# Optimization experiments

Measured on AMD Instinct MI355X. Metric: run time of the kernel, lower is better.

The kernel has to match this reference:

```python
import jax, jax.numpy as jnp
import numpy as np

S, B, D, E, H, REQ = 2048, 4, 256, 256, 8, 16  # seq, batch, hidden_dim, embed(=hidden_size), heads, band half-width


def setup_inputs() -> dict:
    key = jax.random.key(0)
    ks = jax.random.split(key, 12)
    w = lambda k, shape: jax.random.normal(k, shape, jnp.float32) * 0.02
    return {
        "mod": jax.random.normal(ks[0], (S, B, D), jnp.float32),
        "mask": jnp.zeros((B, S), jnp.float32),  # unused in speaker=False branch (kept for fidelity)
        "Wq": w(ks[1], (E, D)), "bq": jnp.zeros((E,), jnp.float32),
        "Wk": w(ks[2], (E, D)), "bk": jnp.zeros((E,), jnp.float32),
        "Wv": w(ks[3], (E, D)), "bv": jnp.zeros((E,), jnp.float32),
        "Win": w(ks[4], (3 * E, E)), "bin_": jnp.zeros((3 * E,), jnp.float32),  # MHA in_proj
        "Wout": w(ks[5], (E, E)), "bout": jnp.zeros((E,), jnp.float32),         # MHA out_proj
        "Wfc": w(ks[6], (D, E)), "bfc": jnp.zeros((D,), jnp.float32),           # self.fc
        "gamma": jnp.ones((D,), jnp.float32), "beta": jnp.zeros((D,), jnp.float32),
        "req": REQ,
    }


def reference(mod, mask, Wq, bq, Wk, bk, Wv, bv, Win, bin_, Wout, bout, Wfc, bfc, gamma, beta, req):
    s, b, d = mod.shape
    e = Wq.shape[0]
    hd = e // H
    # fc_q/k/v (pre-projection) then MultiheadAttention's own in_proj
    q = mod @ Wq.T + bq                       # (s, b, e)
    k = mod @ Wk.T + bk
    v = mod @ Wv.T + bv
    q = q @ Win[:e].T + bin_[:e]
    k = k @ Win[e:2 * e].T + bin_[e:2 * e]
    v = v @ Win[2 * e:].T + bin_[2 * e:]
    split = lambda x: x.reshape(s, b, H, hd).transpose(1, 2, 0, 3)  # (b, H, s, hd)
    qh, kh, vh = split(q), split(k), split(v)
    scores = jnp.einsum('bhqd,bhkd->bhqk', qh, kh) / jnp.sqrt(jnp.float32(hd))
    idx = jnp.arange(s)
    allowed = jnp.abs(idx[:, None] - idx[None, :]) < req  # band: diag + offsets 1..req-1
    scores = jnp.where(allowed[None, None], scores, -jnp.inf)
    attn = jax.nn.softmax(scores, axis=-1)                # attn dropout = identity (eval)
    ctx = jnp.einsum('bhqk,bhkd->bhqd', attn, vh)
    ctx = ctx.transpose(2, 0, 1, 3).reshape(s, b, e)
    ctx = ctx @ Wout.T + bout
    y = ctx @ Wfc.T + bfc + mod                           # dropout(0.5) = identity (eval), residual
    mu = jnp.mean(y, axis=-1, keepdims=True)
    var = jnp.var(y, axis=-1, keepdims=True)
    return (y - mu) / jnp.sqrt(var + 1e-6) * gamma + beta
```

## Files before the change

### kernel.cpp

```cpp
#include <hip/hip_runtime.h>
#include <hip/hip_bf16.h>
#include <math.h>

#define SS 2048
#define BB 4
#define DD 256
#define EE 256
#define HH 8
#define HD 32
#define TT (SS*BB)

typedef unsigned short ushortt;
typedef __attribute__((ext_vector_type(8))) short short8;
typedef __attribute__((ext_vector_type(4))) float f32x4;

__device__ __forceinline__ float bfbits2f(ushortt u) {
    return __uint_as_float(((unsigned int)u) << 16);
}
__device__ __forceinline__ ushortt f2bf_bits(float f) {
    unsigned int u = __float_as_uint(f);
    unsigned int r = u + 0x7FFFu + ((u >> 16) & 1u);
    return (ushortt)(r >> 16);
}

__device__ __forceinline__ int robust_req(const void* p) {
    int i = *(const int*)p;
    if (i >= 1 && i <= SS) return i;
    float f = __int_as_float(i);
    if (f >= 1.f && f <= (float)SS) return (int)(f + 0.5f);
    float b = bfbits2f(*(const ushortt*)p);
    if (b >= 1.f && b <= (float)SS) return (int)(b + 0.5f);
    return 16;
}

__global__ __launch_bounds__(256)
void fuse_weights(const float* __restrict__ Win,
                  const float* __restrict__ Wq, const float* __restrict__ Wk,
                  const float* __restrict__ Wv,
                  const float* __restrict__ bq, const float* __restrict__ bk,
                  const float* __restrict__ bv, const float* __restrict__ bin_,
                  const float* __restrict__ Wfc, const float* __restrict__ Wout,
                  const float* __restrict__ bout, const float* __restrict__ bfc,
                  ushortt* __restrict__ Weffb, float* __restrict__ beff,
                  ushortt* __restrict__ W2b, float* __restrict__ b2) {
    __shared__ float red[4];
    int t = threadIdx.x;
    if (blockIdx.x < 3 * EE) {
        int r = blockIdx.x;
        int i = r / EE;
        const float* Wi = (i == 0) ? Wq : ((i == 1) ? Wk : Wv);
        const float* bi = (i == 0) ? bq : ((i == 1) ? bk : bv);
        float acc = 0.f;
        for (int e1 = 0; e1 < EE; ++e1) acc += Win[r * EE + e1] * Wi[e1 * DD + t];
        Weffb[(size_t)r * DD + t] = f2bf_bits(acc);
        float tb = Win[r * EE + t] * bi[t];
#pragma unroll
        for (int off = 32; off >= 1; off >>= 1) tb += __shfl_xor(tb, off);
        if ((t & 63) == 0) red[t >> 6] = tb;
        __syncthreads();
        if (t == 0) beff[r] = red[0] + red[1] + red[2] + red[3] + bin_[r];
    } else {
        int d = blockIdx.x - 3 * EE;
        float acc = 0.f;
        for (int e = 0; e < EE; ++e) acc += Wfc[d * EE + e] * Wout[e * EE + t];
        W2b[(size_t)d * EE + t] = f2bf_bits(acc);
        float tb = Wfc[d * EE + t] * bout[t];
#pragma unroll
        for (int off = 32; off >= 1; off >>= 1) tb += __shfl_xor(tb, off);
        if ((t & 63) == 0) red[t >> 6] = tb;
        __syncthreads();
        if (t == 0) b2[d] = red[0] + red[1] + red[2] + red[3] + bfc[d];
    }
}

__global__ __launch_bounds__(256)
void gemm_qkv(const float* __restrict__ A, const ushortt* __restrict__ Bw,
              const float* __restrict__ bias, ushortt* __restrict__ C,
              int M, int N, int K) {
    __shared__ __align__(16) ushortt Alds[128][40];
    __shared__ __align__(16) ushortt Blds[64][40];
    const int t    = threadIdx.x;
    const int lane = t & 63;
    const int w    = t >> 6;
    const int wm   = w >> 1, wn = w & 1;
    const int quad = lane >> 4;
    const int l16  = lane & 15;
    const int m0   = blockIdx.y * 128;
    const int n0   = blockIdx.x * 64;

    f32x4 acc[4][2];
#pragma unroll
    for (int fm = 0; fm < 4; ++fm)
#pragma unroll
        for (int fn = 0; fn < 2; ++fn) acc[fm][fn] = (f32x4){0.f, 0.f, 0.f, 0.f};

    const int sr = t >> 2;
    const int sp = (t & 3) * 8;

    for (int k0 = 0; k0 < K; k0 += 32) {
#pragma unroll
        for (int half = 0; half < 2; ++half) {
            const float* ap = A + (size_t)(m0 + sr + half * 64) * K + k0 + sp;
            float4 v0 = *(const float4*)ap;
            float4 v1 = *(const float4*)(ap + 4);
            ushort4 o0, o1;
            o0.x = f2bf_bits(v0.x); o0.y = f2bf_bits(v0.y);
            o0.z = f2bf_bits(v0.z); o0.w = f2bf_bits(v0.w);
            o1.x = f2bf_bits(v1.x); o1.y = f2bf_bits(v1.y);
            o1.z = f2bf_bits(v1.z); o1.w = f2bf_bits(v1.w);
            *(ushort4*)&Alds[sr + half * 64][sp]     = o0;
            *(ushort4*)&Alds[sr + half * 64][sp + 4] = o1;
        }
        *(float4*)&Blds[sr][sp] = *(const float4*)(Bw + (size_t)(n0 + sr) * K + k0 + sp);
        __syncthreads();
        short8 af[4], bfr[2];
#pragma unroll
        for (int fm = 0; fm < 4; ++fm)
            af[fm] = *(const short8*)&Alds[wm * 64 + fm * 16 + l16][quad * 8];
#pragma unroll
        for (int fn = 0; fn < 2; ++fn)
            bfr[fn] = *(const short8*)&Blds[wn * 32 + fn * 16 + l16][quad * 8];
#pragma unroll
        for (int fm = 0; fm < 4; ++fm)
#pragma unroll
            for (int fn = 0; fn < 2; ++fn)
                acc[fm][fn] = __builtin_amdgcn_mfma_f32_16x16x32_bf16(
                    af[fm], bfr[fn], acc[fm][fn], 0, 0, 0);
        __syncthreads();
    }
#pragma unroll
    for (int fm = 0; fm < 4; ++fm)
#pragma unroll
        for (int fn = 0; fn < 2; ++fn)
#pragma unroll
            for (int r = 0; r < 4; ++r) {
                int row = m0 + wm * 64 + fm * 16 + quad * 4 + r;
                int col = n0 + wn * 32 + fn * 16 + l16;
                C[(size_t)row * N + col] = f2bf_bits(acc[fm][fn][r] + bias[col]);
            }
}

__global__ __launch_bounds__(256)
void attn_mfma(const ushortt* __restrict__ qkv,
               const void* __restrict__ reqp,
               ushortt* __restrict__ ctx) {
    __shared__ __align__(16) ushortt Plds[4][16 * 72];
    const int t    = threadIdx.x;
    const int w    = t >> 6;
    const int lane = t & 63;
    const int l16  = lane & 15;
    const int quad = lane >> 4;
    const int wid  = blockIdx.x * 4 + w;
    const int stile = wid >> 5;
    const int rem   = wid & 31;
    const int b = rem >> 3;
    const int h = rem & 7;
    const int s0 = stile * 16;
    const int req = robust_req(reqp);

    const ushortt* qptr = qkv + ((size_t)(s0 + l16) * BB + b) * (3 * EE) + h * HD + quad * 8;
    short8 aq = *(const short8*)qptr;

    f32x4 sc[3];
#pragma unroll
    for (int kt = 0; kt < 3; ++kt) {
        int j = s0 - 16 + kt * 16 + l16;
        int jc = min(max(j, 0), SS - 1);
        const ushortt* kp = qkv + ((size_t)jc * BB + b) * (3 * EE) + EE + h * HD + quad * 8;
        short8 bk = *(const short8*)kp;
        sc[kt] = __builtin_amdgcn_mfma_f32_16x16x32_bf16(aq, bk, (f32x4){0.f,0.f,0.f,0.f}, 0, 0, 0);
    }

    const float scale = 0.17677669529663687f;
    float pv[3][4];
#pragma unroll
    for (int r = 0; r < 4; ++r) {
        int s = s0 + quad * 4 + r;
        float vv[3];
        float mx = -INFINITY;
#pragma unroll
        for (int kt = 0; kt < 3; ++kt) {
            int j = s0 - 16 + kt * 16 + l16;
            int dj = s - j;
            bool valid = (j >= 0) && (j < SS) && (dj < req) && (-dj < req);
            vv[kt] = valid ? sc[kt][r] * scale : -INFINITY;
            mx = fmaxf(mx, vv[kt]);
        }
#pragma unroll
        for (int off = 1; off <= 8; off <<= 1) mx = fmaxf(mx, __shfl_xor(mx, off));
        float sum = 0.f;
#pragma unroll
        for (int kt = 0; kt < 3; ++kt) {
            float p = (vv[kt] > -INFINITY) ? __expf(vv[kt] - mx) : 0.f;
            pv[kt][r] = p;
            sum += p;
        }
#pragma unroll
        for (int off = 1; off <= 8; off <<= 1) sum += __shfl_xor(sum, off);
        float inv = 1.f / sum;
#pragma unroll
        for (int kt = 0; kt < 3; ++kt) pv[kt][r] *= inv;
    }

    ushortt* P = &Plds[w][0];
#pragma unroll
    for (int kt = 0; kt < 3; ++kt)
#pragma unroll
        for (int r = 0; r < 4; ++r)
            P[(quad * 4 + r) * 72 + kt * 16 + l16] = f2bf_bits(pv[kt][r]);
#pragma unroll
    for (int r = 0; r < 4; ++r)
        P[(quad * 4 + r) * 72 + 48 + l16] = 0;
    __syncthreads();

    short8 pa[2];
    pa[0] = *(const short8*)&P[l16 * 72 + quad * 8];
    pa[1] = *(const short8*)&P[l16 * 72 + 32 + quad * 8];

    f32x4 acc[2];
    acc[0] = (f32x4){0.f,0.f,0.f,0.f};
    acc[1] = (f32x4){0.f,0.f,0.f,0.f};
#pragma unroll
    for (int c = 0; c < 2; ++c) {
#pragma unroll
        for (int nd = 0; nd < 2; ++nd) {
            short8 bv;
#pragma unroll
            for (int u = 0; u < 8; ++u) {
                int j = s0 - 16 + c * 32 + quad * 8 + u;
                int jc = min(max(j, 0), SS - 1);
                bv[u] = (short)qkv[((size_t)jc * BB + b) * (3 * EE) + 2 * EE + h * HD + nd * 16 + l16];
            }
            acc[nd] = __builtin_amdgcn_mfma_f32_16x16x32_bf16(pa[c], bv, acc[nd], 0, 0, 0);
        }
    }

#pragma unroll
    for (int nd = 0; nd < 2; ++nd)
#pragma unroll
        for (int r = 0; r < 4; ++r) {
            int tok = (s0 + quad * 4 + r) * BB + b;
            ctx[(size_t)tok * EE + h * HD + nd * 16 + l16] = f2bf_bits(acc[nd][r]);
        }
}

__global__ __launch_bounds__(256)
void gemm_tail_ln(const ushortt* __restrict__ A, const ushortt* __restrict__ Bw,
                  const float* __restrict__ b2, const float* __restrict__ mod,
                  const float* __restrict__ gamma, const float* __restrict__ beta,
                  float* __restrict__ out) {
    __shared__ __align__(16) ushortt Alds[64][40];
    __shared__ __align__(16) ushortt Blds[256][40];
    __shared__ float part1[4][64], part2[4][64];
    const int t    = threadIdx.x;
    const int lane = t & 63;
    const int wn   = t >> 6;
    const int quad = lane >> 4;
    const int l16  = lane & 15;
    const int m0   = blockIdx.x * 64;
    const int N    = DD, K = EE;

    f32x4 acc[4][4];
#pragma unroll
    for (int fm = 0; fm < 4; ++fm)
#pragma unroll
        for (int fn = 0; fn < 4; ++fn) acc[fm][fn] = (f32x4){0.f, 0.f, 0.f, 0.f};

    const int sr = t >> 2;
    const int sp = (t & 3) * 8;

    for (int k0 = 0; k0 < K; k0 += 32) {
        *(float4*)&Alds[sr][sp] = *(const float4*)(A + (size_t)(m0 + sr) * K + k0 + sp);
#pragma unroll
        for (int i = 0; i < 4; ++i)
            *(float4*)&Blds[sr + i * 64][sp] = *(const float4*)(Bw + (size_t)(sr + i * 64) * K + k0 + sp);
        __syncthreads();
        short8 af[4], bfr[4];
#pragma unroll
        for (int fm = 0; fm < 4; ++fm)
            af[fm] = *(const short8*)&Alds[fm * 16 + l16][quad * 8];
#pragma unroll
        for (int fn = 0; fn < 4; ++fn)
            bfr[fn] = *(const short8*)&Blds[wn * 64 + fn * 16 + l16][quad * 8];
#pragma unroll
        for (int fm = 0; fm < 4; ++fm)
#pragma unroll
            for (int fn = 0; fn < 4; ++fn)
                acc[fm][fn] = __builtin_amdgcn_mfma_f32_16x16x32_bf16(
                    af[fm], bfr[fn], acc[fm][fn], 0, 0, 0);
        __syncthreads();
    }

#pragma unroll
    for (int fm = 0; fm < 4; ++fm) {
#pragma unroll
        for (int r = 0; r < 4; ++r) {
            int rowl = fm * 16 + quad * 4 + r;
            int row  = m0 + rowl;
            float s1 = 0.f, s2 = 0.f;
#pragma unroll
            for (int fn = 0; fn < 4; ++fn) {
                int col = wn * 64 + fn * 16 + l16;
                float v = acc[fm][fn][r] + b2[col] + mod[(size_t)row * N + col];
                acc[fm][fn][r] = v;
                s1 += v;
                s2 += v * v;
            }
#pragma unroll
            for (int off = 1; off <= 8; off <<= 1) {
                s1 += __shfl_xor(s1, off);
                s2 += __shfl_xor(s2, off);
            }
            if (l16 == 0) { part1[wn][rowl] = s1; part2[wn][rowl] = s2; }
        }
    }
    __syncthreads();
#pragma unroll
    for (int fm = 0; fm < 4; ++fm) {
#pragma unroll
        for (int r = 0; r < 4; ++r) {
            int rowl = fm * 16 + quad * 4 + r;
            int row  = m0 + rowl;
            float S1 = part1[0][rowl] + part1[1][rowl] + part1[2][rowl] + part1[3][rowl];
            float S2 = part2[0][rowl] + part2[1][rowl] + part2[2][rowl] + part2[3][rowl];
            float mean = S1 * (1.f / DD);
            float var  = S2 * (1.f / DD) - mean * mean;
            float inv  = rsqrtf(var + 1e-6f);
#pragma unroll
            for (int fn = 0; fn < 4; ++fn) {
                int col = wn * 64 + fn * 16 + l16;
                out[(size_t)row * N + col] =
                    (acc[fm][fn][r] - mean) * inv * gamma[col] + beta[col];
            }
        }
    }
}

extern "C" void kernel_launch(void* const* d_in, const int* in_sizes, int n_in,
                              void* d_out, int out_size, void* d_ws, size_t ws_size,
                              hipStream_t stream) {
    const float* mod  = (const float*)d_in[0];
    const float* Wq   = (const float*)d_in[2];
    const float* bq   = (const float*)d_in[3];
    const float* Wk   = (const float*)d_in[4];
    const float* bk   = (const float*)d_in[5];
    const float* Wv   = (const float*)d_in[6];
    const float* bv   = (const float*)d_in[7];
    const float* Win  = (const float*)d_in[8];
    const float* bin_ = (const float*)d_in[9];
    const float* Wout = (const float*)d_in[10];
    const float* bout = (const float*)d_in[11];
    const float* Wfc  = (const float*)d_in[12];
    const float* bfc  = (const float*)d_in[13];
    const float* gamma= (const float*)d_in[14];
    const float* beta = (const float*)d_in[15];
    const void*  reqp = d_in[16];

    float* out = (float*)d_out;

    float*  beff = (float*)d_ws;
    float*  b2   = beff + 3 * EE;
    ushortt* Weffb = (ushortt*)(b2 + DD);
    ushortt* W2b   = Weffb + 3 * EE * DD;
    ushortt* qkvb  = W2b + DD * EE;
    ushortt* ctxb  = qkvb + (size_t)TT * 3 * EE;

    fuse_weights<<<4 * EE, 256, 0, stream>>>(Win, Wq, Wk, Wv, bq, bk, bv, bin_,
                                             Wfc, Wout, bout, bfc,
                                             Weffb, beff, W2b, b2);
    gemm_qkv<<<dim3(3 * EE / 64, TT / 128), 256, 0, stream>>>(
        mod, Weffb, beff, qkvb, TT, 3 * EE, DD);
    attn_mfma<<<4096 / 4, 256, 0, stream>>>(qkvb, reqp, ctxb);
    gemm_tail_ln<<<TT / 64, 256, 0, stream>>>(ctxb, W2b, b2, mod, gamma, beta, out);
}
```

Measured before the change: 141.1 us.

## Fuse all four kernels into one persistent megakernel with software grid barriers

Replaces the four separate launches (weight fusion, QKV GEMM, banded attention, tail GEMM+LayerNorm) with a single persistent kernel of 256 blocks x 512 threads, separated by atomic-counter grid barriers. The aim is to remove per-launch overhead and inter-kernel gaps. The price is smaller GEMM tiles per block, fixed work assignment across 256 blocks, and a spin barrier that relies on all blocks being co-resident and has a timeout break that could silently skip synchronisation. An extra memset is also added for the barrier state.

```diff
diff --git a/kernel.cpp b/kernel.cpp
--- a/kernel.cpp
+++ b/kernel.cpp
@@ -9,6 +9,9 @@
 #define HH 8
 #define HD 32
 #define TT (SS*BB)
+
+#define NBLK 256
+#define NTHR 512
 
 typedef unsigned short ushortt;
 typedef __attribute__((ext_vector_type(8))) short short8;
@@ -33,276 +36,300 @@
     return 16;
 }
 
-__global__ __launch_bounds__(256)
-void fuse_weights(const float* __restrict__ Win,
-                  const float* __restrict__ Wq, const float* __restrict__ Wk,
-                  const float* __restrict__ Wv,
-                  const float* __restrict__ bq, const float* __restrict__ bk,
-                  const float* __restrict__ bv, const float* __restrict__ bin_,
-                  const float* __restrict__ Wfc, const float* __restrict__ Wout,
-                  const float* __restrict__ bout, const float* __restrict__ bfc,
-                  ushortt* __restrict__ Weffb, float* __restrict__ beff,
-                  ushortt* __restrict__ W2b, float* __restrict__ b2) {
-    __shared__ float red[4];
-    int t = threadIdx.x;
-    if (blockIdx.x < 3 * EE) {
-        int r = blockIdx.x;
-        int i = r / EE;
-        const float* Wi = (i == 0) ? Wq : ((i == 1) ? Wk : Wv);
-        const float* bi = (i == 0) ? bq : ((i == 1) ? bk : bv);
-        float acc = 0.f;
-        for (int e1 = 0; e1 < EE; ++e1) acc += Win[r * EE + e1] * Wi[e1 * DD + t];
-        Weffb[(size_t)r * DD + t] = f2bf_bits(acc);
-        float tb = Win[r * EE + t] * bi[t];
-#pragma unroll
-        for (int off = 32; off >= 1; off >>= 1) tb += __shfl_xor(tb, off);
-        if ((t & 63) == 0) red[t >> 6] = tb;
-        __syncthreads();
-        if (t == 0) beff[r] = red[0] + red[1] + red[2] + red[3] + bin_[r];
-    } else {
-        int d = blockIdx.x - 3 * EE;
-        float acc = 0.f;
-        for (int e = 0; e < EE; ++e) acc += Wfc[d * EE + e] * Wout[e * EE + t];
-        W2b[(size_t)d * EE + t] = f2bf_bits(acc);
-        float tb = Wfc[d * EE + t] * bout[t];
-#pragma unroll
-        for (int off = 32; off >= 1; off >>= 1) tb += __shfl_xor(tb, off);
-        if ((t & 63) == 0) red[t >> 6] = tb;
-        __syncthreads();
-        if (t == 0) b2[d] = red[0] + red[1] + red[2] + red[3] + bfc[d];
-    }
-}
-
-__global__ __launch_bounds__(256)
-void gemm_qkv(const float* __restrict__ A, const ushortt* __restrict__ Bw,
-              const float* __restrict__ bias, ushortt* __restrict__ C,
-              int M, int N, int K) {
-    __shared__ __align__(16) ushortt Alds[128][40];
-    __shared__ __align__(16) ushortt Blds[64][40];
+__device__ __forceinline__ void grid_sync(unsigned* cnt, unsigned* gen) {
+    __syncthreads();
+    if (threadIdx.x == 0) {
+        __threadfence();
+        unsigned g = __hip_atomic_load(gen, __ATOMIC_RELAXED, __HIP_MEMORY_SCOPE_AGENT);
+        unsigned a = __hip_atomic_fetch_add(cnt, 1u, __ATOMIC_ACQ_REL, __HIP_MEMORY_SCOPE_AGENT);
+        if (a + 1 == (unsigned)NBLK) {
+            __hip_atomic_store(cnt, 0u, __ATOMIC_RELAXED, __HIP_MEMORY_SCOPE_AGENT);
+            __hip_atomic_store(gen, g + 1u, __ATOMIC_RELEASE, __HIP_MEMORY_SCOPE_AGENT);
+        } else {
+            long long spins = 0;
+            while (__hip_atomic_load(gen, __ATOMIC_ACQUIRE, __HIP_MEMORY_SCOPE_AGENT) == g) {
+                __builtin_amdgcn_s_sleep(2);
+                if (++spins > (1LL << 22)) break;
+            }
+        }
+        __threadfence();
+    }
+    __syncthreads();
+}
+
+__global__ __launch_bounds__(NTHR, 1)
+void mega(const float* __restrict__ mod,
+          const float* __restrict__ Win,
+          const float* __restrict__ Wq, const float* __restrict__ Wk,
+          const float* __restrict__ Wv,
+          const float* __restrict__ bq, const float* __restrict__ bk,
+          const float* __restrict__ bv, const float* __restrict__ bin_,
+          const float* __restrict__ Wfc, const float* __restrict__ Wout,
+          const float* __restrict__ bout, const float* __restrict__ bfc,
+          const float* __restrict__ gamma, const float* __restrict__ beta,
+          const void* __restrict__ reqp,
+          float* __restrict__ beff, float* __restrict__ b2,
+          ushortt* __restrict__ Weffb, ushortt* __restrict__ W2b,
+          ushortt* __restrict__ qkvb, ushortt* __restrict__ ctxb,
+          float* __restrict__ out,
+          unsigned* __restrict__ bar_cnt, unsigned* __restrict__ bar_gen) {
+    __shared__ __align__(16) unsigned char smem[24576];
+
     const int t    = threadIdx.x;
+    const int bid  = blockIdx.x;
+    const int w    = t >> 6;
     const int lane = t & 63;
-    const int w    = t >> 6;
-    const int wm   = w >> 1, wn = w & 1;
     const int quad = lane >> 4;
     const int l16  = lane & 15;
-    const int m0   = blockIdx.y * 128;
-    const int n0   = blockIdx.x * 64;
-
-    f32x4 acc[4][2];
-#pragma unroll
-    for (int fm = 0; fm < 4; ++fm)
-#pragma unroll
-        for (int fn = 0; fn < 2; ++fn) acc[fm][fn] = (f32x4){0.f, 0.f, 0.f, 0.f};
-
-    const int sr = t >> 2;
-    const int sp = (t & 3) * 8;
-
-    for (int k0 = 0; k0 < K; k0 += 32) {
-#pragma unroll
-        for (int half = 0; half < 2; ++half) {
-            const float* ap = A + (size_t)(m0 + sr + half * 64) * K + k0 + sp;
-            float4 v0 = *(const float4*)ap;
-            float4 v1 = *(const float4*)(ap + 4);
-            ushort4 o0, o1;
-            o0.x = f2bf_bits(v0.x); o0.y = f2bf_bits(v0.y);
-            o0.z = f2bf_bits(v0.z); o0.w = f2bf_bits(v0.w);
-            o1.x = f2bf_bits(v1.x); o1.y = f2bf_bits(v1.y);
-            o1.z = f2bf_bits(v1.z); o1.w = f2bf_bits(v1.w);
-            *(ushort4*)&Alds[sr + half * 64][sp]     = o0;
-            *(ushort4*)&Alds[sr + half * 64][sp + 4] = o1;
-        }
-        *(float4*)&Blds[sr][sp] = *(const float4*)(Bw + (size_t)(n0 + sr) * K + k0 + sp);
-        __syncthreads();
-        short8 af[4], bfr[2];
-#pragma unroll
-        for (int fm = 0; fm < 4; ++fm)
-            af[fm] = *(const short8*)&Alds[wm * 64 + fm * 16 + l16][quad * 8];
-#pragma unroll
-        for (int fn = 0; fn < 2; ++fn)
-            bfr[fn] = *(const short8*)&Blds[wn * 32 + fn * 16 + l16][quad * 8];
-#pragma unroll
-        for (int fm = 0; fm < 4; ++fm)
-#pragma unroll
-            for (int fn = 0; fn < 2; ++fn)
-                acc[fm][fn] = __builtin_amdgcn_mfma_f32_16x16x32_bf16(
-                    af[fm], bfr[fn], acc[fm][fn], 0, 0, 0);
-        __syncthreads();
-    }
-#pragma unroll
-    for (int fm = 0; fm < 4; ++fm)
-#pragma unroll
-        for (int fn = 0; fn < 2; ++fn)
+
+    {
+        float* red = (float*)smem;
+        const int half = t >> 8;
+        const int t256 = t & 255;
+#pragma unroll 1
+        for (int rnd = 0; rnd < 2; ++rnd) {
+            int vb = bid * 2 + half + rnd * 512;
+            float tb;
+            if (vb < 3 * EE) {
+                int r = vb;
+                int i = r / EE;
+                const float* Wi = (i == 0) ? Wq : ((i == 1) ? Wk : Wv);
+                const float* bi = (i == 0) ? bq : ((i == 1) ? bk : bv);
+                float acc = 0.f;
+                for (int e1 = 0; e1 < EE; ++e1) acc += Win[r * EE + e1] * Wi[e1 * DD + t256];
+                Weffb[(size_t)r * DD + t256] = f2bf_bits(acc);
+                tb = Win[r * EE + t256] * bi[t256];
+            } else {
+                int d = vb - 3 * EE;
+                float acc = 0.f;
+                for (int e = 0; e < EE; ++e) acc += Wfc[d * EE + e] * Wout[e * EE + t256];
+                W2b[(size_t)d * EE + t256] = f2bf_bits(acc);
+                tb = Wfc[d * EE + t256] * bout[t256];
+            }
+#pragma unroll
+            for (int off = 32; off >= 1; off >>= 1) tb += __shfl_xor(tb, off);
+            if (lane == 0) red[w] = tb;
+            __syncthreads();
+            if (t256 == 0) {
+                float s = red[half * 4] + red[half * 4 + 1] + red[half * 4 + 2] + red[half * 4 + 3];
+                if (vb < 3 * EE) beff[vb] = s + bin_[vb];
+                else             b2[vb - 3 * EE] = s + bfc[vb - 3 * EE];
+            }
+            __syncthreads();
+        }
+    }
+    grid_sync(bar_cnt, bar_gen);
+
+    {
+        ushortt (*Alds)[40] = (ushortt (*)[40])smem;
+        ushortt (*Blds)[40] = (ushortt (*)[40])(smem + 10240);
+        const int wm = w >> 1, wn = w & 1;
+        const int sr = t >> 2;
+        const int sp = (t & 3) * 8;
+#pragma unroll 1
+        for (int i = 0; i < 3; ++i) {
+            int tile = bid + 256 * i;
+            int m0 = (tile / 12) * 128;
+            int n0 = (tile % 12) * 64;
+            f32x4 acc[2][2];
+#pragma unroll
+            for (int fm = 0; fm < 2; ++fm)
+#pragma unroll
+                for (int fn = 0; fn < 2; ++fn) acc[fm][fn] = (f32x4){0.f,0.f,0.f,0.f};
+            for (int k0 = 0; k0 < DD; k0 += 32) {
+                const float* ap = mod + (size_t)(m0 + sr) * DD + k0 + sp;
+                float4 v0 = *(const float4*)ap;
+                float4 v1 = *(const float4*)(ap + 4);
+                ushort4 o0, o1;
+                o0.x = f2bf_bits(v0.x); o0.y = f2bf_bits(v0.y);
+                o0.z = f2bf_bits(v0.z); o0.w = f2bf_bits(v0.w);
+                o1.x = f2bf_bits(v1.x); o1.y = f2bf_bits(v1.y);
+                o1.z = f2bf_bits(v1.z); o1.w = f2bf_bits(v1.w);
+                *(ushort4*)&Alds[sr][sp]     = o0;
+                *(ushort4*)&Alds[sr][sp + 4] = o1;
+                if (t < 256) {
+                    int br = t >> 2;
+                    int bp = (t & 3) * 8;
+                    *(float4*)&Blds[br][bp] =
+                        *(const float4*)(Weffb + (size_t)(n0 + br) * DD + k0 + bp);
+                }
+                __syncthreads();
+                short8 af[2], bfr[2];
+#pragma unroll
+                for (int fm = 0; fm < 2; ++fm)
+                    af[fm] = *(const short8*)&Alds[wm * 32 + fm * 16 + l16][quad * 8];
+#pragma unroll
+                for (int fn = 0; fn < 2; ++fn)
+                    bfr[fn] = *(const short8*)&Blds[wn * 32 + fn * 16 + l16][quad * 8];
+#pragma unroll
+                for (int fm = 0; fm < 2; ++fm)
+#pragma unroll
+                    for (int fn = 0; fn < 2; ++fn)
+                        acc[fm][fn] = __builtin_amdgcn_mfma_f32_16x16x32_bf16(
+                            af[fm], bfr[fn], acc[fm][fn], 0, 0, 0);
+                __syncthreads();
+            }
+#pragma unroll
+            for (int fm = 0; fm < 2; ++fm)
+#pragma unroll
+                for (int fn = 0; fn < 2; ++fn)
+#pragma unroll
+                    for (int r = 0; r < 4; ++r) {
+                        int row = m0 + wm * 32 + fm * 16 + quad * 4 + r;
+                        int col = n0 + wn * 32 + fn * 16 + l16;
+                        qkvb[(size_t)row * (3 * EE) + col] = f2bf_bits(acc[fm][fn][r] + beff[col]);
+                    }
+        }
+    }
+    grid_sync(bar_cnt, bar_gen);
+
+    {
+        ushortt* Pbase = (ushortt*)smem;
+        const int req = robust_req(reqp);
+        const int nk_lo = -(req - 1), nk_hi = req - 1;
+#pragma unroll 1
+        for (int rnd = 0; rnd < 2; ++rnd) {
+            int u = rnd * 2048 + w * 256 + bid;
+            int stile = u >> 5;
+            int rem   = u & 31;
+            int b = rem >> 3;
+            int h = rem & 7;
+            int s0 = stile * 16;
+
+            const ushortt* qptr = qkvb + ((size_t)(s0 + l16) * BB + b) * (3 * EE) + h * HD + quad * 8;
+            short8 aq = *(const short8*)qptr;
+
+            f32x4 sc[3];
+#pragma unroll
+            for (int kt = 0; kt < 3; ++kt) {
+                int j = s0 - 16 + kt * 16 + l16;
+                int jc = min(max(j, 0), SS - 1);
+                const ushortt* kp = qkvb + ((size_t)jc * BB + b) * (3 * EE) + EE + h * HD + quad * 8;
+                short8 bk = *(const short8*)kp;
+                sc[kt] = __builtin_amdgcn_mfma_f32_16x16x32_bf16(aq, bk, (f32x4){0.f,0.f,0.f,0.f}, 0, 0, 0);
+            }
+
+            const float scale = 0.17677669529663687f;
+            float pv[3][4];
 #pragma unroll
             for (int r = 0; r < 4; ++r) {
-                int row = m0 + wm * 64 + fm * 16 + quad * 4 + r;
-                int col = n0 + wn * 32 + fn * 16 + l16;
-                C[(size_t)row * N + col] = f2bf_bits(acc[fm][fn][r] + bias[col]);
-            }
-}
-
-__global__ __launch_bounds__(256)
-void attn_mfma(const ushortt* __restrict__ qkv,
-               const void* __restrict__ reqp,
-               ushortt* __restrict__ ctx) {
-    __shared__ __align__(16) ushortt Plds[4][16 * 72];
-    const int t    = threadIdx.x;
-    const int w    = t >> 6;
-    const int lane = t & 63;
-    const int l16  = lane & 15;
-    const int quad = lane >> 4;
-    const int wid  = blockIdx.x * 4 + w;
-    const int stile = wid >> 5;
-    const int rem   = wid & 31;
-    const int b = rem >> 3;
-    const int h = rem & 7;
-    const int s0 = stile * 16;
-    const int req = robust_req(reqp);
-
-    const ushortt* qptr = qkv + ((size_t)(s0 + l16) * BB + b) * (3 * EE) + h * HD + quad * 8;
-    short8 aq = *(const short8*)qptr;
-
-    f32x4 sc[3];
-#pragma unroll
-    for (int kt = 0; kt < 3; ++kt) {
-        int j = s0 - 16 + kt * 16 + l16;
-        int jc = min(max(j, 0), SS - 1);
-        const ushortt* kp = qkv + ((size_t)jc * BB + b) * (3 * EE) + EE + h * HD + quad * 8;
-        short8 bk = *(const short8*)kp;
-        sc[kt] = __builtin_amdgcn_mfma_f32_16x16x32_bf16(aq, bk, (f32x4){0.f,0.f,0.f,0.f}, 0, 0, 0);
-    }
-
-    const float scale = 0.17677669529663687f;
-    float pv[3][4];
-#pragma unroll
-    for (int r = 0; r < 4; ++r) {
-        int s = s0 + quad * 4 + r;
-        float vv[3];
-        float mx = -INFINITY;
-#pragma unroll
-        for (int kt = 0; kt < 3; ++kt) {
-            int j = s0 - 16 + kt * 16 + l16;
-            int dj = s - j;
-            bool valid = (j >= 0) && (j < SS) && (dj < req) && (-dj < req);
-            vv[kt] = valid ? sc[kt][r] * scale : -INFINITY;
-            mx = fmaxf(mx, vv[kt]);
-        }
-#pragma unroll
-        for (int off = 1; off <= 8; off <<= 1) mx = fmaxf(mx, __shfl_xor(mx, off));
-        float sum = 0.f;
-#pragma unroll
-        for (int kt = 0; kt < 3; ++kt) {
-            float p = (vv[kt] > -INFINITY) ? __expf(vv[kt] - mx) : 0.f;
-            pv[kt][r] = p;
-            sum += p;
-        }
-#pragma unroll
-        for (int off = 1; off <= 8; off <<= 1) sum += __shfl_xor(sum, off);
-        float inv = 1.f / sum;
-#pragma unroll
-        for (int kt = 0; kt < 3; ++kt) pv[kt][r] *= inv;
-    }
-
-    ushortt* P = &Plds[w][0];
-#pragma unroll
-    for (int kt = 0; kt < 3; ++kt)
-#pragma unroll
-        for (int r = 0; r < 4; ++r)
-            P[(quad * 4 + r) * 72 + kt * 16 + l16] = f2bf_bits(pv[kt][r]);
-#pragma unroll
-    for (int r = 0; r < 4; ++r)
-        P[(quad * 4 + r) * 72 + 48 + l16] = 0;
-    __syncthreads();
-
-    short8 pa[2];
-    pa[0] = *(const short8*)&P[l16 * 72 + quad * 8];
-    pa[1] = *(const short8*)&P[l16 * 72 + 32 + quad * 8];
-
-    f32x4 acc[2];
-    acc[0] = (f32x4){0.f,0.f,0.f,0.f};
-    acc[1] = (f32x4){0.f,0.f,0.f,0.f};
-#pragma unroll
-    for (int c = 0; c < 2; ++c) {
-#pragma unroll
-        for (int nd = 0; nd < 2; ++nd) {
-            short8 bv;
-#pragma unroll
-            for (int u = 0; u < 8; ++u) {
-                int j = s0 - 16 + c * 32 + quad * 8 + u;
-                int jc = min(max(j, 0), SS - 1);
-                bv[u] = (short)qkv[((size_t)jc * BB + b) * (3 * EE) + 2 * EE + h * HD + nd * 16 + l16];
-            }
-            acc[nd] = __builtin_amdgcn_mfma_f32_16x16x32_bf16(pa[c], bv, acc[nd], 0, 0, 0);
-        }
-    }
-
-#pragma unroll
-    for (int nd = 0; nd < 2; ++nd)
+                int s = s0 + quad * 4 + r;
+                float vv[3];
+                float mx = -INFINITY;
+#pragma unroll
+                for (int kt = 0; kt < 3; ++kt) {
+                    int j = s0 - 16 + kt * 16 + l16;
+                    int dj = s - j;
+                    bool valid = (j >= 0) && (j < SS) && (dj <= nk_hi) && (dj >= nk_lo);
+                    vv[kt] = valid ? sc[kt][r] * scale : -INFINITY;
+                    mx = fmaxf(mx, vv[kt]);
+                }
+#pragma unroll
+                for (int off = 1; off <= 8; off <<= 1) mx = fmaxf(mx, __shfl_xor(mx, off));
+                float sum = 0.f;
+#pragma unroll
+                for (int kt = 0; kt < 3; ++kt) {
+                    float p = (vv[kt] > -INFINITY) ? __expf(vv[kt] - mx) : 0.f;
+                    pv[kt][r] = p;
+                    sum += p;
+                }
+#pragma unroll
+                for (int off = 1; off <= 8; off <<= 1) sum += __shfl_xor(sum, off);
+                float inv = 1.f / sum;
+#pragma unroll
+                for (int kt = 0; kt < 3; ++kt) pv[kt][r] *= inv;
+            }
+
+            ushortt* P = Pbase + w * (16 * 72);
+#pragma unroll
+            for (int kt = 0; kt < 3; ++kt)
+#pragma unroll
+                for (int r = 0; r < 4; ++r)
+                    P[(quad * 4 + r) * 72 + kt * 16 + l16] = f2bf_bits(pv[kt][r]);
+#pragma unroll
+            for (int r = 0; r < 4; ++r)
+                P[(quad * 4 + r) * 72 + 48 + l16] = 0;
+            __syncthreads();
+
+            short8 pa[2];
+            pa[0] = *(const short8*)&P[l16 * 72 + quad * 8];
+            pa[1] = *(const short8*)&P[l16 * 72 + 32 + quad * 8];
+
+            f32x4 acc2[2];
+            acc2[0] = (f32x4){0.f,0.f,0.f,0.f};
+            acc2[1] = (f32x4){0.f,0.f,0.f,0.f};
+#pragma unroll
+            for (int c = 0; c < 2; ++c) {
+#pragma unroll
+                for (int nd = 0; nd < 2; ++nd) {
+                    short8 bv;
+#pragma unroll
+                    for (int uu = 0; uu < 8; ++uu) {
+                        int j = s0 - 16 + c * 32 + quad * 8 + uu;
+                        int jc = min(max(j, 0), SS - 1);
+                        bv[uu] = (short)qkvb[((size_t)jc * BB + b) * (3 * EE) + 2 * EE + h * HD + nd * 16 + l16];
+                    }
+                    acc2[nd] = __builtin_amdgcn_mfma_f32_16x16x32_bf16(pa[c], bv, acc2[nd], 0, 0, 0);
+                }
+            }
+#pragma unroll
+            for (int nd = 0; nd < 2; ++nd)
+#pragma unroll
+                for (int r = 0; r < 4; ++r) {
+                    int tok = (s0 + quad * 4 + r) * BB + b;
+                    ctxb[(size_t)tok * EE + h * HD + nd * 16 + l16] = f2bf_bits(acc2[nd][r]);
+                }
+            __syncthreads();
+        }
+    }
+    grid_sync(bar_cnt, bar_gen);
+
+    {
+        ushortt (*Alds)[40] = (ushortt (*)[40])smem;
+        ushortt (*Blds)[40] = (ushortt (*)[40])(smem + 2560);
+        float* part1 = (float*)(smem + 23040);
+        float* part2 = (float*)(smem + 23552);
+        const int wm = w >> 2, wn = w & 3;
+        const int t0 = bid * 32;
+
+        f32x4 acc[4];
+#pragma unroll
+        for (int fn = 0; fn < 4; ++fn) acc[fn] = (f32x4){0.f,0.f,0.f,0.f};
+
+        for (int k0 = 0; k0 < EE; k0 += 32) {
+            if (t < 128) {
+                int ar = t >> 2;
+                int ap = (t & 3) * 8;
+                *(float4*)&Alds[ar][ap] = *(const float4*)(ctxb + (size_t)(t0 + ar) * EE + k0 + ap);
+            }
+#pragma unroll
+            for (int i = 0; i < 2; ++i) {
+                int br = (t >> 2) + i * 128;
+                int bp = (t & 3) * 8;
+                *(float4*)&Blds[br][bp] = *(const float4*)(W2b + (size_t)br * EE + k0 + bp);
+            }
+            __syncthreads();
+            short8 af = *(const short8*)&Alds[wm * 16 + l16][quad * 8];
+            short8 bfr[4];
+#pragma unroll
+            for (int fn = 0; fn < 4; ++fn)
+                bfr[fn] = *(const short8*)&Blds[wn * 64 + fn * 16 + l16][quad * 8];
+#pragma unroll
+            for (int fn = 0; fn < 4; ++fn)
+                acc[fn] = __builtin_amdgcn_mfma_f32_16x16x32_bf16(af, bfr[fn], acc[fn], 0, 0, 0);
+            __syncthreads();
+        }
+
 #pragma unroll
         for (int r = 0; r < 4; ++r) {
-            int tok = (s0 + quad * 4 + r) * BB + b;
-            ctx[(size_t)tok * EE + h * HD + nd * 16 + l16] = f2bf_bits(acc[nd][r]);
-        }
-}
-
-__global__ __launch_bounds__(256)
-void gemm_tail_ln(const ushortt* __restrict__ A, const ushortt* __restrict__ Bw,
-                  const float* __restrict__ b2, const float* __restrict__ mod,
-                  const float* __restrict__ gamma, const float* __restrict__ beta,
-                  float* __restrict__ out) {
-    __shared__ __align__(16) ushortt Alds[64][40];
-    __shared__ __align__(16) ushortt Blds[256][40];
-    __shared__ float part1[4][64], part2[4][64];
-    const int t    = threadIdx.x;
-    const int lane = t & 63;
-    const int wn   = t >> 6;
-    const int quad = lane >> 4;
-    const int l16  = lane & 15;
-    const int m0   = blockIdx.x * 64;
-    const int N    = DD, K = EE;
-
-    f32x4 acc[4][4];
-#pragma unroll
-    for (int fm = 0; fm < 4; ++fm)
-#pragma unroll
-        for (int fn = 0; fn < 4; ++fn) acc[fm][fn] = (f32x4){0.f, 0.f, 0.f, 0.f};
-
-    const int sr = t >> 2;
-    const int sp = (t & 3) * 8;
-
-    for (int k0 = 0; k0 < K; k0 += 32) {
-        *(float4*)&Alds[sr][sp] = *(const float4*)(A + (size_t)(m0 + sr) * K + k0 + sp);
-#pragma unroll
-        for (int i = 0; i < 4; ++i)
-            *(float4*)&Blds[sr + i * 64][sp] = *(const float4*)(Bw + (size_t)(sr + i * 64) * K + k0 + sp);
-        __syncthreads();
-        short8 af[4], bfr[4];
-#pragma unroll
-        for (int fm = 0; fm < 4; ++fm)
-            af[fm] = *(const short8*)&Alds[fm * 16 + l16][quad * 8];
-#pragma unroll
-        for (int fn = 0; fn < 4; ++fn)
-            bfr[fn] = *(const short8*)&Blds[wn * 64 + fn * 16 + l16][quad * 8];
-#pragma unroll
-        for (int fm = 0; fm < 4; ++fm)
-#pragma unroll
-            for (int fn = 0; fn < 4; ++fn)
-                acc[fm][fn] = __builtin_amdgcn_mfma_f32_16x16x32_bf16(
-                    af[fm], bfr[fn], acc[fm][fn], 0, 0, 0);
-        __syncthreads();
-    }
-
-#pragma unroll
-    for (int fm = 0; fm < 4; ++fm) {
-#pragma unroll
-        for (int r = 0; r < 4; ++r) {
-            int rowl = fm * 16 + quad * 4 + r;
-            int row  = m0 + rowl;
+            int rowl = wm * 16 + quad * 4 + r;
+            int row  = t0 + rowl;
             float s1 = 0.f, s2 = 0.f;
 #pragma unroll
             for (int fn = 0; fn < 4; ++fn) {
                 int col = wn * 64 + fn * 16 + l16;
-                float v = acc[fm][fn][r] + b2[col] + mod[(size_t)row * N + col];
-                acc[fm][fn][r] = v;
+                float v = acc[fn][r] + b2[col] + mod[(size_t)row * DD + col];
+                acc[fn][r] = v;
                 s1 += v;
                 s2 += v * v;
             }
@@ -311,26 +338,22 @@
                 s1 += __shfl_xor(s1, off);
                 s2 += __shfl_xor(s2, off);
             }
-            if (l16 == 0) { part1[wn][rowl] = s1; part2[wn][rowl] = s2; }
-        }
-    }
-    __syncthreads();
-#pragma unroll
-    for (int fm = 0; fm < 4; ++fm) {
+            if (l16 == 0) { part1[wn * 32 + rowl] = s1; part2[wn * 32 + rowl] = s2; }
+        }
+        __syncthreads();
 #pragma unroll
         for (int r = 0; r < 4; ++r) {
-            int rowl = fm * 16 + quad * 4 + r;
-            int row  = m0 + rowl;
-            float S1 = part1[0][rowl] + part1[1][rowl] + part1[2][rowl] + part1[3][rowl];
-            float S2 = part2[0][rowl] + part2[1][rowl] + part2[2][rowl] + part2[3][rowl];
+            int rowl = wm * 16 + quad * 4 + r;
+            int row  = t0 + rowl;
+            float S1 = part1[rowl] + part1[32 + rowl] + part1[64 + rowl] + part1[96 + rowl];
+            float S2 = part2[rowl] + part2[32 + rowl] + part2[64 + rowl] + part2[96 + rowl];
             float mean = S1 * (1.f / DD);
             float var  = S2 * (1.f / DD) - mean * mean;
             float inv  = rsqrtf(var + 1e-6f);
 #pragma unroll
             for (int fn = 0; fn < 4; ++fn) {
                 int col = wn * 64 + fn * 16 + l16;
-                out[(size_t)row * N + col] =
-                    (acc[fm][fn][r] - mean) * inv * gamma[col] + beta[col];
+                out[(size_t)row * DD + col] = (acc[fn][r] - mean) * inv * gamma[col] + beta[col];
             }
         }
     }
@@ -364,12 +387,13 @@
     ushortt* W2b   = Weffb + 3 * EE * DD;
     ushortt* qkvb  = W2b + DD * EE;
     ushortt* ctxb  = qkvb + (size_t)TT * 3 * EE;
-
-    fuse_weights<<<4 * EE, 256, 0, stream>>>(Win, Wq, Wk, Wv, bq, bk, bv, bin_,
-                                             Wfc, Wout, bout, bfc,
-                                             Weffb, beff, W2b, b2);
-    gemm_qkv<<<dim3(3 * EE / 64, TT / 128), 256, 0, stream>>>(
-        mod, Weffb, beff, qkvb, TT, 3 * EE, DD);
-    attn_mfma<<<4096 / 4, 256, 0, stream>>>(qkvb, reqp, ctxb);
-    gemm_tail_ln<<<TT / 64, 256, 0, stream>>>(ctxb, W2b, b2, mod, gamma, beta, out);
-}
+    unsigned* bar  = (unsigned*)((char*)d_ws + (32u << 20));
+    unsigned* bar_cnt = bar;
+    unsigned* bar_gen = bar + 1;
+
+    hipMemsetAsync((void*)bar, 0, 256, stream);
+    mega<<<NBLK, NTHR, 0, stream>>>(mod, Win, Wq, Wk, Wv, bq, bk, bv, bin_,
+                                    Wfc, Wout, bout, bfc, gamma, beta, reqp,
+                                    beff, b2, Weffb, W2b, qkvb, ctxb, out,
+                                    bar_cnt, bar_gen);
+}
```

Result: slower. 276.8 us (+96.2%).

## Pre-convert mod to bf16 in weight-fusion kernel and retile both GEMMs

Applied to the files above, without the earlier changes.

The weight-fusion kernel now also converts the fp32 input activations to bf16 in a workspace buffer, so the QKV GEMM loads bf16 directly instead of converting per tile. The QKV GEMM switches to 64x192 tiles with a K-step of 64, and the tail GEMM+LayerNorm uses 32-row tiles with a K-step of 64, doubling its grid size. The aim is fewer K-loop iterations and barriers, less redundant conversion, and more blocks for the tail kernel. The cost is an extra bf16 write and read of the activations and more LDS per block, with the weight tiles reloaded by more blocks.

```diff
diff --git a/kernel.cpp b/kernel.cpp
--- a/kernel.cpp
+++ b/kernel.cpp
@@ -34,17 +34,34 @@
 }
 
 __global__ __launch_bounds__(256)
-void fuse_weights(const float* __restrict__ Win,
-                  const float* __restrict__ Wq, const float* __restrict__ Wk,
-                  const float* __restrict__ Wv,
-                  const float* __restrict__ bq, const float* __restrict__ bk,
-                  const float* __restrict__ bv, const float* __restrict__ bin_,
-                  const float* __restrict__ Wfc, const float* __restrict__ Wout,
-                  const float* __restrict__ bout, const float* __restrict__ bfc,
-                  ushortt* __restrict__ Weffb, float* __restrict__ beff,
-                  ushortt* __restrict__ W2b, float* __restrict__ b2) {
+void fuse_conv(const float* __restrict__ mod,
+               const float* __restrict__ Win,
+               const float* __restrict__ Wq, const float* __restrict__ Wk,
+               const float* __restrict__ Wv,
+               const float* __restrict__ bq, const float* __restrict__ bk,
+               const float* __restrict__ bv, const float* __restrict__ bin_,
+               const float* __restrict__ Wfc, const float* __restrict__ Wout,
+               const float* __restrict__ bout, const float* __restrict__ bfc,
+               ushortt* __restrict__ Weffb, float* __restrict__ beff,
+               ushortt* __restrict__ W2b, float* __restrict__ b2,
+               ushortt* __restrict__ modb) {
     __shared__ float red[4];
-    int t = threadIdx.x;
+    const int t = threadIdx.x;
+
+    {
+        size_t base = (size_t)blockIdx.x * 2048 + (size_t)t * 8;
+        float4 v0 = *(const float4*)(mod + base);
+        float4 v1 = *(const float4*)(mod + base + 4);
+        ushort4 o0, o1;
+        o0.x = f2bf_bits(v0.x); o0.y = f2bf_bits(v0.y);
+        o0.z = f2bf_bits(v0.z); o0.w = f2bf_bits(v0.w);
+        o1.x = f2bf_bits(v1.x); o1.y = f2bf_bits(v1.y);
+        o1.z = f2bf_bits(v1.z); o1.w = f2bf_bits(v1.w);
+        *(ushort4*)(modb + base)     = o0;
+        *(ushort4*)(modb + base + 4) = o1;
+    }
+
+    float tb;
     if (blockIdx.x < 3 * EE) {
         int r = blockIdx.x;
         int i = r / EE;
@@ -53,89 +70,88 @@
         float acc = 0.f;
         for (int e1 = 0; e1 < EE; ++e1) acc += Win[r * EE + e1] * Wi[e1 * DD + t];
         Weffb[(size_t)r * DD + t] = f2bf_bits(acc);
-        float tb = Win[r * EE + t] * bi[t];
-#pragma unroll
-        for (int off = 32; off >= 1; off >>= 1) tb += __shfl_xor(tb, off);
-        if ((t & 63) == 0) red[t >> 6] = tb;
-        __syncthreads();
-        if (t == 0) beff[r] = red[0] + red[1] + red[2] + red[3] + bin_[r];
+        tb = Win[r * EE + t] * bi[t];
     } else {
         int d = blockIdx.x - 3 * EE;
         float acc = 0.f;
         for (int e = 0; e < EE; ++e) acc += Wfc[d * EE + e] * Wout[e * EE + t];
         W2b[(size_t)d * EE + t] = f2bf_bits(acc);
-        float tb = Wfc[d * EE + t] * bout[t];
-#pragma unroll
-        for (int off = 32; off >= 1; off >>= 1) tb += __shfl_xor(tb, off);
-        if ((t & 63) == 0) red[t >> 6] = tb;
-        __syncthreads();
-        if (t == 0) b2[d] = red[0] + red[1] + red[2] + red[3] + bfc[d];
+        tb = Wfc[d * EE + t] * bout[t];
+    }
+#pragma unroll
+    for (int off = 32; off >= 1; off >>= 1) tb += __shfl_xor(tb, off);
+    if ((t & 63) == 0) red[t >> 6] = tb;
+    __syncthreads();
+    if (t == 0) {
+        float s = red[0] + red[1] + red[2] + red[3];
+        if (blockIdx.x < 3 * EE) beff[blockIdx.x] = s + bin_[blockIdx.x];
+        else                     b2[blockIdx.x - 3 * EE] = s + bfc[blockIdx.x - 3 * EE];
     }
 }
 
 __global__ __launch_bounds__(256)
-void gemm_qkv(const float* __restrict__ A, const ushortt* __restrict__ Bw,
-              const float* __restrict__ bias, ushortt* __restrict__ C,
-              int M, int N, int K) {
-    __shared__ __align__(16) ushortt Alds[128][40];
-    __shared__ __align__(16) ushortt Blds[64][40];
+void gemm_qkv(const ushortt* __restrict__ A, const ushortt* __restrict__ Bw,
+              const float* __restrict__ bias, ushortt* __restrict__ C) {
+    __shared__ __align__(16) ushortt Alds[64][72];
+    __shared__ __align__(16) ushortt Blds[192][72];
     const int t    = threadIdx.x;
     const int lane = t & 63;
     const int w    = t >> 6;
-    const int wm   = w >> 1, wn = w & 1;
     const int quad = lane >> 4;
     const int l16  = lane & 15;
-    const int m0   = blockIdx.y * 128;
-    const int n0   = blockIdx.x * 64;
-
-    f32x4 acc[4][2];
+    const int n0   = blockIdx.x * 192;
+    const int m0   = blockIdx.y * 64;
+    const int N    = 3 * EE, K = DD;
+
+    f32x4 acc[4][3];
 #pragma unroll
     for (int fm = 0; fm < 4; ++fm)
 #pragma unroll
-        for (int fn = 0; fn < 2; ++fn) acc[fm][fn] = (f32x4){0.f, 0.f, 0.f, 0.f};
-
-    const int sr = t >> 2;
-    const int sp = (t & 3) * 8;
-
-    for (int k0 = 0; k0 < K; k0 += 32) {
-#pragma unroll
-        for (int half = 0; half < 2; ++half) {
-            const float* ap = A + (size_t)(m0 + sr + half * 64) * K + k0 + sp;
-            float4 v0 = *(const float4*)ap;
-            float4 v1 = *(const float4*)(ap + 4);
-            ushort4 o0, o1;
-            o0.x = f2bf_bits(v0.x); o0.y = f2bf_bits(v0.y);
-            o0.z = f2bf_bits(v0.z); o0.w = f2bf_bits(v0.w);
-            o1.x = f2bf_bits(v1.x); o1.y = f2bf_bits(v1.y);
-            o1.z = f2bf_bits(v1.z); o1.w = f2bf_bits(v1.w);
-            *(ushort4*)&Alds[sr + half * 64][sp]     = o0;
-            *(ushort4*)&Alds[sr + half * 64][sp + 4] = o1;
-        }
-        *(float4*)&Blds[sr][sp] = *(const float4*)(Bw + (size_t)(n0 + sr) * K + k0 + sp);
+        for (int fn = 0; fn < 3; ++fn) acc[fm][fn] = (f32x4){0.f,0.f,0.f,0.f};
+
+    for (int k0 = 0; k0 < K; k0 += 64) {
+        {
+            int row = t >> 2, c8 = (t & 3) * 8;
+            const ushortt* ap = A + (size_t)(m0 + row) * K + k0;
+            *(float4*)&Alds[row][c8]      = *(const float4*)(ap + c8);
+            *(float4*)&Alds[row][c8 + 32] = *(const float4*)(ap + c8 + 32);
+        }
+#pragma unroll
+        for (int i = 0; i < 6; ++i) {
+            int slot = t + 256 * i;
+            int row = slot >> 3, c8 = (slot & 7) * 8;
+            *(float4*)&Blds[row][c8] = *(const float4*)(Bw + (size_t)(n0 + row) * K + k0 + c8);
+        }
         __syncthreads();
-        short8 af[4], bfr[2];
+        short8 af[4][2], bfr[3][2];
 #pragma unroll
         for (int fm = 0; fm < 4; ++fm)
-            af[fm] = *(const short8*)&Alds[wm * 64 + fm * 16 + l16][quad * 8];
-#pragma unroll
-        for (int fn = 0; fn < 2; ++fn)
-            bfr[fn] = *(const short8*)&Blds[wn * 32 + fn * 16 + l16][quad * 8];
-#pragma unroll
-        for (int fm = 0; fm < 4; ++fm)
-#pragma unroll
-            for (int fn = 0; fn < 2; ++fn)
-                acc[fm][fn] = __builtin_amdgcn_mfma_f32_16x16x32_bf16(
-                    af[fm], bfr[fn], acc[fm][fn], 0, 0, 0);
+#pragma unroll
+            for (int kf = 0; kf < 2; ++kf)
+                af[fm][kf] = *(const short8*)&Alds[fm * 16 + l16][kf * 32 + quad * 8];
+#pragma unroll
+        for (int fn = 0; fn < 3; ++fn)
+#pragma unroll
+            for (int kf = 0; kf < 2; ++kf)
+                bfr[fn][kf] = *(const short8*)&Blds[w * 48 + fn * 16 + l16][kf * 32 + quad * 8];
+#pragma unroll
+        for (int kf = 0; kf < 2; ++kf)
+#pragma unroll
+            for (int fm = 0; fm < 4; ++fm)
+#pragma unroll
+                for (int fn = 0; fn < 3; ++fn)
+                    acc[fm][fn] = __builtin_amdgcn_mfma_f32_16x16x32_bf16(
+                        af[fm][kf], bfr[fn][kf], acc[fm][fn], 0, 0, 0);
         __syncthreads();
     }
 #pragma unroll
     for (int fm = 0; fm < 4; ++fm)
 #pragma unroll
-        for (int fn = 0; fn < 2; ++fn)
+        for (int fn = 0; fn < 3; ++fn)
 #pragma unroll
             for (int r = 0; r < 4; ++r) {
-                int row = m0 + wm * 64 + fm * 16 + quad * 4 + r;
-                int col = n0 + wn * 32 + fn * 16 + l16;
+                int row = m0 + fm * 16 + quad * 4 + r;
+                int col = n0 + w * 48 + fn * 16 + l16;
                 C[(size_t)row * N + col] = f2bf_bits(acc[fm][fn][r] + bias[col]);
             }
 }
@@ -249,50 +265,59 @@
                   const float* __restrict__ b2, const float* __restrict__ mod,
                   const float* __restrict__ gamma, const float* __restrict__ beta,
                   float* __restrict__ out) {
-    __shared__ __align__(16) ushortt Alds[64][40];
-    __shared__ __align__(16) ushortt Blds[256][40];
-    __shared__ float part1[4][64], part2[4][64];
+    __shared__ __align__(16) ushortt Alds[32][72];
+    __shared__ __align__(16) ushortt Blds[256][72];
+    __shared__ float part1[4][32], part2[4][32];
     const int t    = threadIdx.x;
     const int lane = t & 63;
-    const int wn   = t >> 6;
+    const int w    = t >> 6;
     const int quad = lane >> 4;
     const int l16  = lane & 15;
-    const int m0   = blockIdx.x * 64;
-    const int N    = DD, K = EE;
-
-    f32x4 acc[4][4];
-#pragma unroll
-    for (int fm = 0; fm < 4; ++fm)
-#pragma unroll
-        for (int fn = 0; fn < 4; ++fn) acc[fm][fn] = (f32x4){0.f, 0.f, 0.f, 0.f};
-
-    const int sr = t >> 2;
-    const int sp = (t & 3) * 8;
-
-    for (int k0 = 0; k0 < K; k0 += 32) {
-        *(float4*)&Alds[sr][sp] = *(const float4*)(A + (size_t)(m0 + sr) * K + k0 + sp);
-#pragma unroll
-        for (int i = 0; i < 4; ++i)
-            *(float4*)&Blds[sr + i * 64][sp] = *(const float4*)(Bw + (size_t)(sr + i * 64) * K + k0 + sp);
+    const int m0   = blockIdx.x * 32;
+    const int K    = EE;
+
+    f32x4 acc[2][4];
+#pragma unroll
+    for (int fm = 0; fm < 2; ++fm)
+#pragma unroll
+        for (int fn = 0; fn < 4; ++fn) acc[fm][fn] = (f32x4){0.f,0.f,0.f,0.f};
+
+    for (int k0 = 0; k0 < K; k0 += 64) {
+        {
+            int row = t >> 3, c8 = (t & 7) * 8;
+            *(float4*)&Alds[row][c8] = *(const float4*)(A + (size_t)(m0 + row) * K + k0 + c8);
+        }
+#pragma unroll
+        for (int i = 0; i < 8; ++i) {
+            int slot = t + 256 * i;
+            int row = slot >> 3, c8 = (slot & 7) * 8;
+            *(float4*)&Blds[row][c8] = *(const float4*)(Bw + (size_t)row * K + k0 + c8);
+        }
         __syncthreads();
-        short8 af[4], bfr[4];
-#pragma unroll
-        for (int fm = 0; fm < 4; ++fm)
-            af[fm] = *(const short8*)&Alds[fm * 16 + l16][quad * 8];
+        short8 af[2][2], bfr[4][2];
+#pragma unroll
+        for (int fm = 0; fm < 2; ++fm)
+#pragma unroll
+            for (int kf = 0; kf < 2; ++kf)
+                af[fm][kf] = *(const short8*)&Alds[fm * 16 + l16][kf * 32 + quad * 8];
 #pragma unroll
         for (int fn = 0; fn < 4; ++fn)
-            bfr[fn] = *(const short8*)&Blds[wn * 64 + fn * 16 + l16][quad * 8];
-#pragma unroll
-        for (int fm = 0; fm < 4; ++fm)
-#pragma unroll
-            for (int fn = 0; fn < 4; ++fn)
-                acc[fm][fn] = __builtin_amdgcn_mfma_f32_16x16x32_bf16(
-                    af[fm], bfr[fn], acc[fm][fn], 0, 0, 0);
+#pragma unroll
+            for (int kf = 0; kf < 2; ++kf)
+                bfr[fn][kf] = *(const short8*)&Blds[w * 64 + fn * 16 + l16][kf * 32 + quad * 8];
+#pragma unroll
+        for (int kf = 0; kf < 2; ++kf)
+#pragma unroll
+            for (int fm = 0; fm < 2; ++fm)
+#pragma unroll
+                for (int fn = 0; fn < 4; ++fn)
+                    acc[fm][fn] = __builtin_amdgcn_mfma_f32_16x16x32_bf16(
+                        af[fm][kf], bfr[fn][kf], acc[fm][fn], 0, 0, 0);
         __syncthreads();
     }
 
 #pragma unroll
-    for (int fm = 0; fm < 4; ++fm) {
+    for (int fm = 0; fm < 2; ++fm) {
 #pragma unroll
         for (int r = 0; r < 4; ++r) {
             int rowl = fm * 16 + quad * 4 + r;
@@ -300,8 +325,8 @@
             float s1 = 0.f, s2 = 0.f;
 #pragma unroll
             for (int fn = 0; fn < 4; ++fn) {
-                int col = wn * 64 + fn * 16 + l16;
-                float v = acc[fm][fn][r] + b2[col] + mod[(size_t)row * N + col];
+                int col = w * 64 + fn * 16 + l16;
+                float v = acc[fm][fn][r] + b2[col] + mod[(size_t)row * DD + col];
                 acc[fm][fn][r] = v;
                 s1 += v;
                 s2 += v * v;
@@ -311,12 +336,12 @@
                 s1 += __shfl_xor(s1, off);
                 s2 += __shfl_xor(s2, off);
             }
-            if (l16 == 0) { part1[wn][rowl] = s1; part2[wn][rowl] = s2; }
+            if (l16 == 0) { part1[w][rowl] = s1; part2[w][rowl] = s2; }
         }
     }
     __syncthreads();
 #pragma unroll
-    for (int fm = 0; fm < 4; ++fm) {
+    for (int fm = 0; fm < 2; ++fm) {
 #pragma unroll
         for (int r = 0; r < 4; ++r) {
             int rowl = fm * 16 + quad * 4 + r;
@@ -328,9 +353,8 @@
             float inv  = rsqrtf(var + 1e-6f);
 #pragma unroll
             for (int fn = 0; fn < 4; ++fn) {
-                int col = wn * 64 + fn * 16 + l16;
-                out[(size_t)row * N + col] =
-                    (acc[fm][fn][r] - mean) * inv * gamma[col] + beta[col];
+                int col = w * 64 + fn * 16 + l16;
+                out[(size_t)row * DD + col] = (acc[fm][fn][r] - mean) * inv * gamma[col] + beta[col];
             }
         }
     }
@@ -362,14 +386,14 @@
     float*  b2   = beff + 3 * EE;
     ushortt* Weffb = (ushortt*)(b2 + DD);
     ushortt* W2b   = Weffb + 3 * EE * DD;
-    ushortt* qkvb  = W2b + DD * EE;
+    ushortt* modb  = W2b + DD * EE;
+    ushortt* qkvb  = modb + (size_t)TT * DD;
     ushortt* ctxb  = qkvb + (size_t)TT * 3 * EE;
 
-    fuse_weights<<<4 * EE, 256, 0, stream>>>(Win, Wq, Wk, Wv, bq, bk, bv, bin_,
-                                             Wfc, Wout, bout, bfc,
-                                             Weffb, beff, W2b, b2);
-    gemm_qkv<<<dim3(3 * EE / 64, TT / 128), 256, 0, stream>>>(
-        mod, Weffb, beff, qkvb, TT, 3 * EE, DD);
+    fuse_conv<<<1024, 256, 0, stream>>>(mod, Win, Wq, Wk, Wv, bq, bk, bv, bin_,
+                                        Wfc, Wout, bout, bfc,
+                                        Weffb, beff, W2b, b2, modb);
+    gemm_qkv<<<dim3(4, TT / 64), 256, 0, stream>>>(modb, Weffb, beff, qkvb);
     attn_mfma<<<4096 / 4, 256, 0, stream>>>(qkvb, reqp, ctxb);
-    gemm_tail_ln<<<TT / 64, 256, 0, stream>>>(ctxb, W2b, b2, mod, gamma, beta, out);
-}
+    gemm_tail_ln<<<TT / 32, 256, 0, stream>>>(ctxb, W2b, b2, mod, gamma, beta, out);
+}
```

New measurement: 129.4 us. -8.3%, faster.
